# Performance work log

Measured on AMD Instinct MI355X. Metric: run time of the kernel, lower is better.

The kernel has to match this reference:

```python
import jax, jax.numpy as jnp
from jax import lax
import numpy as np

NUM_CLASSES = 21
CONF_THR = 0.01
NMS_THR = 0.45
TOP_K = 200
KEEP_TOP_K = 200
MIN_SIZES = [30., 60., 111., 162., 213., 264.]
MAX_SIZES = [60., 111., 162., 213., 264., 315.]
ASPECT_RATIOS = [[2.], [2., 3.], [2., 3.], [2., 3.], [2.], [2.]]
STEPS = [8., 16., 32., 64., 100., 300.]
VARIANCE = np.array([0.1, 0.1, 0.2, 0.2], np.float32)
CHANNELS = [512, 1024, 512, 256, 256, 256]
FEAT_HW = [38, 19, 10, 5, 3, 1]
IMG = 300.0
BATCH = 32


def _make_priors(i):
    # Caffe-style PriorBox: per cell -> [min, sqrt(min*max), ar & flipped ar boxes]
    fh = fw = FEAT_HW[i]
    m, M, step = MIN_SIZES[i], MAX_SIZES[i], STEPS[i]
    wh = [(m, m), (np.sqrt(m * M), np.sqrt(m * M))]
    for ar in ASPECT_RATIOS[i]:
        r = np.sqrt(ar)
        wh.append((m * r, m / r))
        wh.append((m / r, m * r))  # flip
    wh = np.asarray(wh, np.float32)                       # [np, 2]
    ys, xs = np.meshgrid(np.arange(fh), np.arange(fw), indexing='ij')
    cx = ((xs + 0.5) * step / IMG).astype(np.float32)     # [fh, fw]
    cy = ((ys + 0.5) * step / IMG).astype(np.float32)
    w = wh[:, 0] / IMG
    h = wh[:, 1] / IMG
    xmin = cx[..., None] - w * 0.5                        # [fh, fw, np]
    ymin = cy[..., None] - h * 0.5
    xmax = cx[..., None] + w * 0.5
    ymax = cy[..., None] + h * 0.5
    return np.stack([xmin, ymin, xmax, ymax], -1).reshape(-1, 4)


def _conv2d(x, w, b):
    y = lax.conv_general_dilated(x, w, (1, 1), 'SAME',
                                 dimension_numbers=('NCHW', 'OIHW', 'NCHW'))
    return y + b[None, :, None, None]


def _decode(loc, pri):
    # CENTER_SIZE decode with variance not encoded in target
    pw = pri[:, 2] - pri[:, 0]
    ph = pri[:, 3] - pri[:, 1]
    pcx = (pri[:, 0] + pri[:, 2]) * 0.5
    pcy = (pri[:, 1] + pri[:, 3]) * 0.5
    cx = pcx + VARIANCE[0] * loc[..., 0] * pw
    cy = pcy + VARIANCE[1] * loc[..., 1] * ph
    w = pw * jnp.exp(VARIANCE[2] * loc[..., 2])
    h = ph * jnp.exp(VARIANCE[3] * loc[..., 3])
    return jnp.stack([cx - w * 0.5, cy - h * 0.5, cx + w * 0.5, cy + h * 0.5], -1)


def _pairwise_iou(b):
    x1 = jnp.maximum(b[:, None, 0], b[None, :, 0])
    y1 = jnp.maximum(b[:, None, 1], b[None, :, 1])
    x2 = jnp.minimum(b[:, None, 2], b[None, :, 2])
    y2 = jnp.minimum(b[:, None, 3], b[None, :, 3])
    inter = jnp.clip(x2 - x1, 0.) * jnp.clip(y2 - y1, 0.)
    area = (b[:, 2] - b[:, 0]) * (b[:, 3] - b[:, 1])
    union = area[:, None] + area[None, :] - inter
    return inter / jnp.maximum(union, 1e-9)


def _nms_keep(iou, valid, thr):
    # sequential greedy suppression on score-sorted boxes (scan over rows)
    K = iou.shape[0]
    order = jnp.arange(K)
    def step(keep, i):
        sup = (iou[i] > thr) & (order > i) & keep[i]
        return keep & ~sup, None
    keep, _ = lax.scan(step, valid, order)
    return keep


def _per_image(boxes, conf, img_id):
    # boxes [P,4], conf [P,C]
    cls_scores = conf[:, 1:].T  # [C-1, P] (skip background class 0)
    def per_class(sc):
        s = jnp.where(sc > CONF_THR, sc, 0.)
        ts, idx = lax.top_k(s, TOP_K)
        b = boxes[idx]
        keep = _nms_keep(_pairwise_iou(b), ts > 0., NMS_THR)
        return jnp.where(keep, ts, 0.), b
    sc, bx = jax.vmap(per_class)(cls_scores)           # [C-1,K], [C-1,K,4]
    labels = jnp.repeat(jnp.arange(1, NUM_CLASSES), TOP_K).astype(jnp.float32)
    fs = sc.reshape(-1)
    fb = bx.reshape(-1, 4)
    ks, ki = lax.top_k(fs, KEEP_TOP_K)
    kb = fb[ki]
    kl = jnp.where(ks > 0., labels[ki], -1.)
    img_col = jnp.full((KEEP_TOP_K, 1), img_id, jnp.float32)
    return jnp.concatenate([img_col, kl[:, None], ks[:, None], kb], axis=1)  # [K,7]


PRIORS = jnp.asarray(np.concatenate([_make_priors(i) for i in range(6)], 0))  # [8732,4]


def setup_inputs():
    key = jax.random.key(0)
    ks = iter(jax.random.split(key, 64))
    d = {}
    for i, (c, hw) in enumerate(zip(CHANNELS, FEAT_HW)):
        d[f"feat{i}"] = jax.random.normal(next(ks), (BATCH, c, hw, hw), jnp.float32)
    d["img_tensor"] = jax.random.normal(next(ks), (BATCH, 3, 300, 300), jnp.float32)
    for i, c in enumerate(CHANNELS):
        npc = 2 + 2 * len(ASPECT_RATIOS[i])
        d[f"loc_w{i}"] = jax.random.normal(next(ks), (npc * 4, c, 3, 3), jnp.float32) * 0.01
        d[f"loc_b{i}"] = jnp.zeros((npc * 4,), jnp.float32)
        d[f"conf_w{i}"] = jax.random.normal(next(ks), (npc * NUM_CLASSES, c, 3, 3), jnp.float32) * 0.01
        d[f"conf_b{i}"] = jnp.zeros((npc * NUM_CLASSES,), jnp.float32)
    return d


def reference(feat0, feat1, feat2, feat3, feat4, feat5, img_tensor,
              loc_w0, loc_b0, conf_w0, conf_b0,
              loc_w1, loc_b1, conf_w1, conf_b1,
              loc_w2, loc_b2, conf_w2, conf_b2,
              loc_w3, loc_b3, conf_w3, conf_b3,
              loc_w4, loc_b4, conf_w4, conf_b4,
              loc_w5, loc_b5, conf_w5, conf_b5):
    feats = [feat0, feat1, feat2, feat3, feat4, feat5]
    lw = [loc_w0, loc_w1, loc_w2, loc_w3, loc_w4, loc_w5]
    lb = [loc_b0, loc_b1, loc_b2, loc_b3, loc_b4, loc_b5]
    cw = [conf_w0, conf_w1, conf_w2, conf_w3, conf_w4, conf_w5]
    cb = [conf_b0, conf_b1, conf_b2, conf_b3, conf_b4, conf_b5]
    B = feats[0].shape[0]
    locs, confs = [], []
    for i in range(6):
        # conv head -> NHWC -> flat, matching permute(0,2,3,1).view(B,-1)
        locs.append(_conv2d(feats[i], lw[i], lb[i]).transpose(0, 2, 3, 1).reshape(B, -1))
        confs.append(_conv2d(feats[i], cw[i], cb[i]).transpose(0, 2, 3, 1).reshape(B, -1))
    loc = jnp.concatenate(locs, 1).reshape(B, -1, 4)                       # [B,P,4]
    conf = jax.nn.softmax(jnp.concatenate(confs, 1).reshape(B, -1, NUM_CLASSES), -1)
    boxes = _decode(loc, PRIORS)                                           # [B,P,4]
    return jax.vmap(_per_image)(boxes, conf, jnp.arange(B, dtype=jnp.float32))  # [B,200,7]
```

## Files before the change

kernel.cpp:

```cpp
#include <hip/hip_runtime.h>
#include <math.h>

#define BATCH 32
#define P_TOTAL 8732


typedef __attribute__((ext_vector_type(8))) short bf16x8;
typedef __attribute__((ext_vector_type(4))) float f32x4;
typedef unsigned int uint;
typedef unsigned short ushort;

struct SQ {
  int C, logC, H, W, HW, M, ksteps, NL, N, npc, pbase, blkBase;
  int aOffB, wpkOffB, pauxOffB, biasOffB;
};
struct WPtrs { const float* lw[6]; const float* lb[6]; const float* cw[6]; const float* cb[6]; };
struct Tables { SQ sq[6]; int fillBase[6]; int fillTotal; int biasBase[6]; int biasTotal; };

__device__ __forceinline__ ushort f2bf(float f) {
  uint u = __float_as_uint(f);
  return (ushort)((u + 0x7FFFu + ((u >> 16) & 1u)) >> 16);
}
__device__ __forceinline__ float bf2f(ushort b) { return __uint_as_float(((uint)b) << 16); }

__global__ void make_priors(float* __restrict__ priors) {
  int p = blockIdx.x * 256 + threadIdx.x;
  if (p >= P_TOTAL) return;
  const int pb1 = 5776, pb2 = 7942, pb3 = 8542, pb4 = 8692, pb5 = 8728;
  int base, fw, npc;
  double m, M, st;
  if (p < pb1)      { base = 0;   fw = 38; npc = 4; m = 30.;  M = 60.;  st = 8.;   }
  else if (p < pb2) { base = pb1; fw = 19; npc = 6; m = 60.;  M = 111.; st = 16.;  }
  else if (p < pb3) { base = pb2; fw = 10; npc = 6; m = 111.; M = 162.; st = 32.;  }
  else if (p < pb4) { base = pb3; fw = 5;  npc = 6; m = 162.; M = 213.; st = 64.;  }
  else if (p < pb5) { base = pb4; fw = 3;  npc = 4; m = 213.; M = 264.; st = 100.; }
  else              { base = pb5; fw = 1;  npc = 4; m = 264.; M = 315.; st = 300.; }
  int lp = p - base;
  int cell = lp / npc, j = lp - cell * npc;
  int y = cell / fw, x = cell - y * fw;
  double w_, h_;
  if (j == 0)      { w_ = m; h_ = m; }
  else if (j == 1) { double ss = sqrt(m * M); w_ = ss; h_ = ss; }
  else {
    int q = j - 2;
    double r = sqrt((q < 2) ? 2.0 : 3.0);
    if ((q & 1) == 0) { w_ = m * r; h_ = m / r; }
    else              { w_ = m / r; h_ = m * r; }
  }
  float wf = (float)w_ / 300.0f;
  float hf = (float)h_ / 300.0f;
  float cx = (float)(((double)x + 0.5) * st / 300.0);
  float cy = (float)(((double)y + 0.5) * st / 300.0);
  float4 pr;
  pr.x = cx - wf * 0.5f; pr.y = cy - hf * 0.5f;
  pr.z = cx + wf * 0.5f; pr.w = cy + hf * 0.5f;
  ((float4*)priors)[p] = pr;
}

__global__ void nchw_to_nhwc(const float* __restrict__ in, float* __restrict__ out,
                             int C, int HW) {
  __shared__ float tile[32][33];
  int b = blockIdx.z;
  int hw0 = blockIdx.x * 32;
  int c0 = blockIdx.y * 32;
  int tx = threadIdx.x;
  int ty = threadIdx.y;
  const float* ip = in + (size_t)b * C * HW;
  float* op = out + (size_t)b * C * HW;
#pragma unroll
  for (int r = 0; r < 4; ++r) {
    int c = c0 + ty + 8 * r;
    int hw = hw0 + tx;
    tile[ty + 8 * r][tx] = (c < C && hw < HW) ? ip[(size_t)c * HW + hw] : 0.f;
  }
  __syncthreads();
#pragma unroll
  for (int r = 0; r < 4; ++r) {
    int hw = hw0 + ty + 8 * r;
    int c = c0 + tx;
    if (c < C && hw < HW) op[(size_t)hw * C + c] = tile[tx][ty + 8 * r];
  }
}

__global__ void zero_ws(uint4* __restrict__ p, long n) {
  uint4 z; z.x = z.y = z.z = z.w = 0u;
  for (long i = (long)blockIdx.x * 256 + threadIdx.x; i < n; i += (long)gridDim.x * 256)
    p[i] = z;
}

__global__ void wpk_fill(WPtrs wp, Tables tb, char* __restrict__ wsb) {
  int e = blockIdx.x * 256 + threadIdx.x;
  if (e >= tb.fillTotal) return;
  int s = 0;
#pragma unroll
  for (int i = 1; i < 6; ++i) if (e >= tb.fillBase[i]) s = i;
  SQ q = tb.sq[s];
  int le = e - tb.fillBase[s];
  int C8 = q.C >> 3;
  int n = le / C8, co = (le - n * C8) * 8;
  const float* src = (n < q.NL) ? (wp.lw[s] + ((size_t)n * q.C + co) * 9)
                                : (wp.cw[s] + ((size_t)(n - q.NL) * q.C + co) * 9);
  float v[72];
#pragma unroll
  for (int i = 0; i < 72; ++i) v[i] = src[i];
  int f = n >> 4, ln = n & 15;
  int g = (co & 31) >> 3;
  int NF = (q.N + 15) >> 4;
  char* wbase = wsb + q.wpkOffB;
#pragma unroll
  for (int tap = 0; tap < 9; ++tap) {
    int kb = (tap * q.C + co) >> 5;
    ushort h0[8], h1[8], h2[8];
#pragma unroll
    for (int i = 0; i < 8; ++i) {
      float a = v[i * 9 + tap];
      ushort a0 = f2bf(a); float t = a - bf2f(a0);
      ushort a1 = f2bf(t); float t2 = t - bf2f(a1);
      ushort a2 = f2bf(t2);
      h0[i] = a0; h1[i] = a1; h2[i] = a2;
    }
    char* d = wbase + (size_t)kb * NF * 3072 + f * 3072 + (g * 16 + ln) * 16;
    *(uint4*)(d)        = *(uint4*)h0;
    *(uint4*)(d + 1024) = *(uint4*)h1;
    *(uint4*)(d + 2048) = *(uint4*)h2;
  }
}

__global__ void bias_fill(WPtrs wp, Tables tb, char* __restrict__ wsb) {
  int e = blockIdx.x * 256 + threadIdx.x;
  if (e >= tb.biasTotal) return;
  int s = 0;
#pragma unroll
  for (int i = 1; i < 6; ++i) if (e >= tb.biasBase[i]) s = i;
  SQ q = tb.sq[s];
  int ln = e - tb.biasBase[s];
  float v = 0.f;
  if (ln < q.N) v = (ln < q.NL) ? wp.lb[s][ln] : wp.cb[s][ln - q.NL];
  ((float*)(wsb + q.biasOffB))[ln] = v;
}

__device__ __forceinline__ void split8(const float* vv, uint4& o0, uint4& o1, uint4& o2) {
  uint* a = (uint*)&o0; uint* b = (uint*)&o1; uint* c = (uint*)&o2;
#pragma unroll
  for (int i = 0; i < 4; ++i) {
    float x = vv[2 * i], y = vv[2 * i + 1];
    ushort x0 = f2bf(x); float xr = x - bf2f(x0);
    ushort x1 = f2bf(xr); ushort x2 = f2bf(xr - bf2f(x1));
    ushort y0 = f2bf(y); float yr = y - bf2f(y0);
    ushort y1 = f2bf(yr); ushort y2 = f2bf(yr - bf2f(y1));
    a[i] = (uint)x0 | ((uint)y0 << 16);
    b[i] = (uint)x1 | ((uint)y1 << 16);
    c[i] = (uint)x2 | ((uint)y2 << 16);
  }
}

template<int NF, bool PART>
__global__ __launch_bounds__(256, 2) void conv_mfma(const char* __restrict__ wsb,
                                                    SQ q0, SQ q1, SQ q2,
                                                    float* __restrict__ locbuf,
                                                    float* __restrict__ confbuf) {
  __shared__ char sm[30720 + NF * 3072];
  const int bid = blockIdx.x;
  SQ q = (bid >= q2.blkBase) ? q2 : ((bid >= q1.blkBase) ? q1 : q0);
  const int tid = threadIdx.x;
  const int C = q.C, W = q.W, H = q.H, HW = q.HW, M = q.M;
  int lb = bid - q.blkBase;
  int m0, kbeg, kend;
  if (PART) {
    m0 = (lb >> 1) * 128;
    int ks2 = q.ksteps >> 1;
    kbeg = (lb & 1) * ks2; kend = kbeg + ks2;
  } else {
    m0 = lb * 128; kbeg = 0; kend = q.ksteps;
  }
  const float* Amat = (const float*)(wsb + q.aOffB);
  const char* wpk = wsb + q.wpkOffB;

  const int r0 = tid >> 2, oct = tid & 3;
  int ry[2], rx[2], rrow[2];
  bool rv[2];
#pragma unroll
  for (int h = 0; h < 2; ++h) {
    int m = m0 + r0 + 64 * h;
    bool v = m < M;
    int mc = v ? m : 0;
    int b = mc / HW, rem = mc - b * HW;
    ry[h] = rem / W; rx[h] = rem - ry[h] * W; rrow[h] = b * H; rv[h] = v;
  }

  f32x4 cb[2][NF], ct[2][NF];
#pragma unroll
  for (int rf = 0; rf < 2; ++rf)
#pragma unroll
    for (int f = 0; f < NF; ++f) { cb[rf][f] = 0.f; ct[rf][f] = 0.f; }

  const int lane = tid & 63, wv = tid >> 6;
  const int ksub = q.logC - 5, kmask = (1 << ksub) - 1;
  int abase[2];
#pragma unroll
  for (int rf = 0; rf < 2; ++rf)
    abase[rf] = (32 * wv + 16 * rf + (lane & 15)) * 80 + (lane >> 4) * 16;

  for (int kb = kbeg; kb < kend; ++kb) {
    int tap = kb >> ksub;
    int c0 = (kb & kmask) << 5;
    int t3 = tap * 21846 >> 16;
    int dy = t3 - 1, dx = tap - t3 * 3 - 1;
    __syncthreads();
#pragma unroll
    for (int h = 0; h < 2; ++h) {
      int iy = ry[h] + dy, ix = rx[h] + dx;
      bool ok = rv[h] && (unsigned)iy < (unsigned)H && (unsigned)ix < (unsigned)W;
      float4 f0, f1;
      f0.x = f0.y = f0.z = f0.w = 0.f; f1 = f0;
      if (ok) {
        const float* p = Amat + (size_t)((rrow[h] + iy) * W + ix) * C + c0 + oct * 8;
        f0 = ((const float4*)p)[0]; f1 = ((const float4*)p)[1];
      }
      float vv[8] = {f0.x, f0.y, f0.z, f0.w, f1.x, f1.y, f1.z, f1.w};
      uint4 o0, o1, o2;
      split8(vv, o0, o1, o2);
      int ab = (r0 + 64 * h) * 80 + oct * 16;
      *(uint4*)(sm + ab)         = o0;
      *(uint4*)(sm + 10240 + ab) = o1;
      *(uint4*)(sm + 20480 + ab) = o2;
    }
    {
      const char* wsrc = wpk + (size_t)kb * (NF * 3072);
#pragma unroll
      for (int j = 0; j < (NF * 192 + 255) / 256; ++j) {
        int c = tid + j * 256;
        if (c < NF * 192) *(uint4*)(sm + 30720 + c * 16) = *(const uint4*)(wsrc + c * 16);
      }
    }
    __syncthreads();
    bf16x8 a0[2], a1[2], a2[2];
#pragma unroll
    for (int rf = 0; rf < 2; ++rf) {
      a0[rf] = *(const bf16x8*)(sm + abase[rf]);
      a1[rf] = *(const bf16x8*)(sm + 10240 + abase[rf]);
      a2[rf] = *(const bf16x8*)(sm + 20480 + abase[rf]);
    }
#pragma unroll
    for (int f = 0; f < NF; ++f) {
      const char* bp = sm + 30720 + f * 3072 + lane * 16;
      bf16x8 b0 = *(const bf16x8*)(bp);
      bf16x8 b1 = *(const bf16x8*)(bp + 1024);
      bf16x8 b2 = *(const bf16x8*)(bp + 2048);
#pragma unroll
      for (int rf = 0; rf < 2; ++rf) {
        cb[rf][f] = __builtin_amdgcn_mfma_f32_16x16x32_bf16(a0[rf], b0, cb[rf][f], 0, 0, 0);
        cb[rf][f] = __builtin_amdgcn_mfma_f32_16x16x32_bf16(a1[rf], b0, cb[rf][f], 0, 0, 0);
        cb[rf][f] = __builtin_amdgcn_mfma_f32_16x16x32_bf16(a0[rf], b1, cb[rf][f], 0, 0, 0);
        cb[rf][f] = __builtin_amdgcn_mfma_f32_16x16x32_bf16(a1[rf], b1, cb[rf][f], 0, 0, 0);
        cb[rf][f] = __builtin_amdgcn_mfma_f32_16x16x32_bf16(a2[rf], b0, cb[rf][f], 0, 0, 0);
        cb[rf][f] = __builtin_amdgcn_mfma_f32_16x16x32_bf16(a0[rf], b2, cb[rf][f], 0, 0, 0);
      }
    }
    if (((kb - kbeg) & 15) == 15 || kb == kend - 1) {
#pragma unroll
      for (int rf = 0; rf < 2; ++rf)
#pragma unroll
        for (int f = 0; f < NF; ++f) { ct[rf][f] += cb[rf][f]; cb[rf][f] = 0.f; }
    }
  }

  const float* bias = (const float*)(wsb + q.biasOffB);
#pragma unroll
  for (int rf = 0; rf < 2; ++rf) {
#pragma unroll
    for (int f = 0; f < NF; ++f) {
      int n = 16 * f + (lane & 15);
      if (n >= q.N) continue;
      int mrow = m0 + 32 * wv + 16 * rf + 4 * (lane >> 4);
      if (PART) {
        float* paux = (float*)(wsb + q.pauxOffB);
#pragma unroll
        for (int r = 0; r < 4; ++r) {
          int m = mrow + r;
          if (m < M) atomicAdd(&paux[(long)m * 160 + n], ct[rf][f][r]);
        }
      } else {
        float bv = bias[n];
#pragma unroll
        for (int r = 0; r < 4; ++r) {
          int m = mrow + r;
          if (m >= M) continue;
          float v = ct[rf][f][r] + bv;
          int b = m / HW, rem = m - b * HW;
          int pidx0 = q.pbase + rem * q.npc;
          if (n < q.NL) {
            locbuf[((long)b * P_TOTAL + pidx0 + (n >> 2)) * 4 + (n & 3)] = v;
          } else {
            int cn = n - q.NL;
            int pr = cn / 21, cl = cn - pr * 21;
            confbuf[((long)b * P_TOTAL + pidx0 + pr) * 21 + cl] = v;
          }
        }
      }
    }
  }
}

__global__ __launch_bounds__(256) void epi2(const char* __restrict__ wsb,
                                            SQ qa, SQ qb, SQ qc, int ta, int tb, int total,
                                            float* __restrict__ locbuf,
                                            float* __restrict__ confbuf) {
  int e = blockIdx.x * 256 + threadIdx.x;
  if (e >= total) return;
  SQ q; int le;
  if (e < ta) { q = qa; le = e; }
  else if (e < tb) { q = qb; le = e - ta; }
  else { q = qc; le = e - tb; }
  int m = le / q.N, n = le - m * q.N;
  float v = ((const float*)(wsb + q.pauxOffB))[(long)m * 160 + n]
          + ((const float*)(wsb + q.biasOffB))[n];
  int b = m / q.HW, rem = m - b * q.HW;
  int pidx0 = q.pbase + rem * q.npc;
  if (n < q.NL) {
    locbuf[((long)b * P_TOTAL + pidx0 + (n >> 2)) * 4 + (n & 3)] = v;
  } else {
    int cn = n - q.NL;
    int pr = cn / 21, cl = cn - pr * 21;
    confbuf[((long)b * P_TOTAL + pidx0 + pr) * 21 + cl] = v;
  }
}

__global__ __launch_bounds__(256) void decode_softmax(const float* __restrict__ locbuf,
                                                      const float* __restrict__ confbuf,
                                                      const float* __restrict__ priors,
                                                      float* __restrict__ boxes,
                                                      float* __restrict__ scores_t) {
  __shared__ float sc[20 * 256];
  int b = blockIdx.y;
  int p0 = blockIdx.x * 256;
  int tid = threadIdx.x;
  int p = p0 + tid;
  if (p < P_TOTAL) {
    long t = (long)b * P_TOTAL + p;
    float4 pri = ((const float4*)priors)[p];
    float4 lo = ((const float4*)locbuf)[t];
    float pw = pri.z - pri.x, ph = pri.w - pri.y;
    float pcx = (pri.x + pri.z) * 0.5f, pcy = (pri.y + pri.w) * 0.5f;
    float cx = pcx + 0.1f * lo.x * pw;
    float cy = pcy + 0.1f * lo.y * ph;
    float w = pw * expf(0.2f * lo.z);
    float h = ph * expf(0.2f * lo.w);
    float4 bx;
    bx.x = cx - w * 0.5f; bx.y = cy - h * 0.5f;
    bx.z = cx + w * 0.5f; bx.w = cy + h * 0.5f;
    ((float4*)boxes)[t] = bx;
    const float* cp = confbuf + t * 21;
    float l[21];
#pragma unroll
    for (int c = 0; c < 21; ++c) l[c] = cp[c];
    float mx = l[0];
#pragma unroll
    for (int c = 1; c < 21; ++c) mx = fmaxf(mx, l[c]);
    float e[21];
    float sum = 0.f;
#pragma unroll
    for (int c = 0; c < 21; ++c) { e[c] = expf(l[c] - mx); sum += e[c]; }
#pragma unroll
    for (int c = 1; c < 21; ++c) sc[(c - 1) * 256 + tid] = e[c] / sum;
  } else {
#pragma unroll
    for (int c = 0; c < 20; ++c) sc[c * 256 + tid] = 0.f;
  }
  __syncthreads();
  int np = min(256, P_TOTAL - p0);
  if (tid < np) {
    for (int c = 0; c < 20; ++c)
      scores_t[((long)b * 20 + c) * P_TOTAL + p0 + tid] = sc[c * 256 + tid];
  }
}

__global__ __launch_bounds__(256) void topk_nms(const float* __restrict__ scores_t,
                                                const float* __restrict__ boxes,
                                                float* __restrict__ pc_scores,
                                                float* __restrict__ pc_boxes) {
  int bc = blockIdx.x;
  int b = bc / 20;
  int tid = threadIdx.x;
  const float* sp = scores_t + (long)bc * P_TOTAL;

  float vals[35];
#pragma unroll
  for (int u = 0; u < 35; ++u) {
    int idx = u * 256 + tid;
    float v = -1.f;
    if (idx < P_TOTAL) {
      float s = sp[idx];
      v = (s > 0.01f) ? s : 0.f;
    }
    vals[u] = v;
  }

  __shared__ unsigned long long wred[4];
  __shared__ unsigned long long winner;
  __shared__ int sel_idx[200];
  __shared__ float sel_sc[200];
  __shared__ float bX1[200], bY1[200], bX2[200], bY2[200], bAr[200];

  for (int r = 0; r < 200; ++r) {
    float bv = vals[0]; int bu = 0;
#pragma unroll
// ... 60 lines not shown
            float yy1 = fmaxf(iy1, my1[s2]);
            float xx2 = fminf(ix2, mx2[s2]);
            float yy2 = fminf(iy2, my2[s2]);
            float inter = fmaxf(xx2 - xx1, 0.f) * fmaxf(yy2 - yy1, 0.f);
            float uni = fmaxf(ia + ma[s2] - inter, 1e-9f);
            if (inter / uni > 0.45f) km &= ~(1u << s2);
          }
        }
      }
    }
#pragma unroll
    for (int s2 = 0; s2 < 4; ++s2) {
      int j = tid + 64 * s2;
      if (j < 200) {
        long o = (long)bc * 200 + j;
        pc_scores[o] = ((km >> s2) & 1) ? sel_sc[j] : 0.f;
        float4 ob; ob.x = mx1[s2]; ob.y = my1[s2]; ob.z = mx2[s2]; ob.w = my2[s2];
        ((float4*)pc_boxes)[o] = ob;
      }
    }
  }
}

__global__ __launch_bounds__(256) void final_topk(const float* __restrict__ pc_scores,
                                                  const float* __restrict__ pc_boxes,
                                                  float* __restrict__ out) {
  int b = blockIdx.x;
  int tid = threadIdx.x;
  const float* fs = pc_scores + (long)b * 4000;
  float vals[16];
#pragma unroll
  for (int u = 0; u < 16; ++u) {
    int idx = u * 256 + tid;
    vals[u] = (idx < 4000) ? fs[idx] : -1.f;
  }
  __shared__ unsigned long long wred[4];
  __shared__ unsigned long long winner;
  __shared__ int kidx[200];
  __shared__ float ksc[200];
  for (int r = 0; r < 200; ++r) {
    float bv = vals[0]; int bu = 0;
#pragma unroll
    for (int u = 1; u < 16; ++u)
      if (vals[u] > bv) { bv = vals[u]; bu = u; }
    int bidx = bu * 256 + tid;
    unsigned long long key = (bv < 0.f) ? 0ull
        : (((unsigned long long)__float_as_uint(bv) << 32) | (unsigned)(0x7FFFFFFF - bidx));
#pragma unroll
    for (int off = 32; off > 0; off >>= 1) {
      unsigned long long o = __shfl_down(key, off);
      if (o > key) key = o;
    }
    if ((tid & 63) == 0) wred[tid >> 6] = key;
    __syncthreads();
    if (tid == 0) {
      unsigned long long k0 = wred[0];
      for (int w = 1; w < 4; ++w) if (wred[w] > k0) k0 = wred[w];
      winner = k0;
      kidx[r] = 0x7FFFFFFF - (int)(unsigned)(k0 & 0xFFFFFFFFu);
      ksc[r] = __uint_as_float((unsigned)(k0 >> 32));
    }
    __syncthreads();
    int wi = 0x7FFFFFFF - (int)(unsigned)(winner & 0xFFFFFFFFu);
    if ((wi & 255) == tid) {
      int u = wi >> 8;
#pragma unroll
      for (int uu = 0; uu < 16; ++uu) if (uu == u) vals[uu] = -1.f;
    }
    __syncthreads();
  }
  if (tid < 200) {
    int j = kidx[tid];
    float sc2 = ksc[tid];
    float4 bx = ((const float4*)pc_boxes)[(long)b * 4000 + j];
    float lab = (sc2 > 0.f) ? (float)(1 + j / 200) : -1.f;
    long o = ((long)b * 200 + tid) * 7;
    out[o + 0] = (float)b;
    out[o + 1] = lab;
    out[o + 2] = sc2;
    out[o + 3] = bx.x; out[o + 4] = bx.y; out[o + 5] = bx.z; out[o + 6] = bx.w;
  }
}

extern "C" void kernel_launch(void* const* d_in, const int* in_sizes, int n_in,
                              void* d_out, int out_size, void* d_ws, size_t ws_size,
                              hipStream_t stream) {
  (void)in_sizes; (void)n_in; (void)out_size; (void)ws_size;
  static const int CH[6]   = {512, 1024, 512, 256, 256, 256};
  static const int LOGC[6] = {9, 10, 9, 8, 8, 8};
  static const int FHW[6]  = {38, 19, 10, 5, 3, 1};
  static const int NPC[6]  = {4, 6, 6, 6, 4, 4};
  char* wsb = (char*)d_ws;
  Tables tb;
  WPtrs wp;
  auto al = [](size_t v) { return (v + 255) & ~(size_t)255; };
  size_t off = 0;
  int pb = 0;
  for (int s = 0; s < 6; ++s) {
    SQ& q = tb.sq[s];
    q.C = CH[s]; q.logC = LOGC[s]; q.H = FHW[s]; q.W = FHW[s];
    q.HW = FHW[s] * FHW[s];
    q.M = BATCH * q.HW;
    q.ksteps = CH[s] * 9 / 32;
    q.npc = NPC[s]; q.NL = NPC[s] * 4; q.N = NPC[s] * 25;
    q.pbase = pb; pb += q.HW * q.npc;
    q.aOffB = (int)off; off = al(off + (size_t)BATCH * q.HW * q.C * 4);
  }
  size_t zeroStart = off;
  for (int s = 0; s < 6; ++s) {
    int NF = (tb.sq[s].N + 15) >> 4;
    tb.sq[s].wpkOffB = (int)off;
    off = al(off + (size_t)tb.sq[s].ksteps * NF * 3072);
  }
  for (int s = 1; s <= 3; ++s) {
    tb.sq[s].pauxOffB = (int)off;
    off = al(off + (size_t)tb.sq[s].M * 160 * 4);
  }
  tb.sq[0].pauxOffB = tb.sq[4].pauxOffB = tb.sq[5].pauxOffB = 0;
  size_t zeroEnd = off;
  for (int s = 0; s < 6; ++s) {
    int NF = (tb.sq[s].N + 15) >> 4;
    tb.sq[s].biasOffB = (int)off;
    off = al(off + (size_t)NF * 16 * 4);
  }
  size_t priorsOffB = off; off = al(off + (size_t)P_TOTAL * 16);
  size_t locOffB    = off; off = al(off + (size_t)BATCH * P_TOTAL * 16);
  size_t confOffB   = off; off = al(off + (size_t)BATCH * P_TOTAL * 21 * 4);
  size_t boxesOffB  = off; off = al(off + (size_t)BATCH * P_TOTAL * 16);
  size_t scTOffB    = off; off = al(off + (size_t)BATCH * 20 * P_TOTAL * 4);
  size_t pcScOffB   = off; off = al(off + (size_t)BATCH * 20 * 200 * 4);
  size_t pcBxOffB   = off; off = al(off + (size_t)BATCH * 20 * 200 * 16);

  int fb = 0, bb = 0;
  for (int s = 0; s < 6; ++s) {
    tb.fillBase[s] = fb; fb += tb.sq[s].N * (tb.sq[s].C >> 3);
    tb.biasBase[s] = bb; bb += ((tb.sq[s].N + 15) >> 4) * 16;
  }
  tb.fillTotal = fb;
  tb.biasTotal = bb;

  for (int s = 0; s < 6; ++s) {
    wp.lw[s] = (const float*)d_in[7 + 4 * s];
    wp.lb[s] = (const float*)d_in[8 + 4 * s];
    wp.cw[s] = (const float*)d_in[9 + 4 * s];
    wp.cb[s] = (const float*)d_in[10 + 4 * s];
  }

  float* priors   = (float*)(wsb + priorsOffB);
  float* locbuf   = (float*)(wsb + locOffB);
  float* confbuf  = (float*)(wsb + confOffB);
  float* boxes    = (float*)(wsb + boxesOffB);
  float* scores_t = (float*)(wsb + scTOffB);
  float* pcSc     = (float*)(wsb + pcScOffB);
  float* pcBx     = (float*)(wsb + pcBxOffB);

  make_priors<<<(P_TOTAL + 255) / 256, 256, 0, stream>>>(priors);

  for (int s = 0; s < 6; ++s) {
    int hw = FHW[s] * FHW[s];
    dim3 g((hw + 31) / 32, (CH[s] + 31) / 32, BATCH);
    nchw_to_nhwc<<<g, dim3(32, 8), 0, stream>>>((const float*)d_in[s],
                                                (float*)(wsb + tb.sq[s].aOffB), CH[s], hw);
  }

  long zn = (long)((zeroEnd - zeroStart) >> 4);
  zero_ws<<<4096, 256, 0, stream>>>((uint4*)(wsb + zeroStart), zn);

  wpk_fill<<<(tb.fillTotal + 255) / 256, 256, 0, stream>>>(wp, tb, wsb);
  bias_fill<<<(tb.biasTotal + 255) / 256, 256, 0, stream>>>(wp, tb, wsb);

  {
    SQ q0 = tb.sq[0], q1 = tb.sq[4], q2 = tb.sq[5];
    q0.blkBase = 0;
    q1.blkBase = (q0.M + 127) / 128;
    q2.blkBase = q1.blkBase + (q1.M + 127) / 128;
    int grid = q2.blkBase + (q2.M + 127) / 128;
    conv_mfma<7, false><<<grid, 256, 0, stream>>>(wsb, q0, q1, q2, locbuf, confbuf);
  }
  {
    SQ q0 = tb.sq[1], q1 = tb.sq[2], q2 = tb.sq[3];
    q0.blkBase = 0;
    q1.blkBase = 2 * ((q0.M + 127) / 128);
    q2.blkBase = q1.blkBase + 2 * ((q1.M + 127) / 128);
    int grid = q2.blkBase + 2 * ((q2.M + 127) / 128);
    conv_mfma<10, true><<<grid, 256, 0, stream>>>(wsb, q0, q1, q2, locbuf, confbuf);
    int ta = q0.M * q0.N;
    int tbv = ta + q1.M * q1.N;
    int total = tbv + q2.M * q2.N;
    epi2<<<(total + 255) / 256, 256, 0, stream>>>(wsb, q0, q1, q2, ta, tbv, total,
                                                  locbuf, confbuf);
  }

  decode_softmax<<<dim3(35, BATCH), 256, 0, stream>>>(locbuf, confbuf, priors, boxes, scores_t);

  topk_nms<<<BATCH * 20, 256, 0, stream>>>(scores_t, boxes, pcSc, pcBx);

  final_topk<<<BATCH, 256, 0, stream>>>(pcSc, pcBx, (float*)d_out);
}
```

Baseline: 1.799 ms.

## Pre-split activations into bf16 planes and double-buffer weights in conv pipeline

The NCHW-to-NHWC transpose now also splits activations into three bf16 planes, so the MFMA conv kernel reads A fragments straight from global memory and no longer does per-step fp32 loads, splitting and shared-memory staging. Weight tiles are register-prefetched and double-buffered in shared memory, which removes one barrier per k-step. The split-K partial sums go to per-part buffers and are reduced by a single epilogue for all scales, which removes the atomics and the zeroing pass. The change also merges the bias fill into wpk_fill, uses magic-number divisions, splits K more finely for some scales, and reuses workspace regions. The cost is three times the activation-plane footprint and more global traffic for uncoalesced A loads.

Measured after the change: 2.075 ms. 1.15x slower.

```diff
diff --git a/kernel.cpp b/kernel.cpp
--- a/kernel.cpp
+++ b/kernel.cpp
@@ -11,11 +11,14 @@
 typedef unsigned short ushort;
 
 struct SQ {
-  int C, logC, H, W, HW, M, ksteps, NL, N, npc, pbase, blkBase;
-  int aOffB, wpkOffB, pauxOffB, biasOffB;
+  int C, H, W, HW, M, NL, N, npc, pbase;
+  int chunks, parts, mtiles, blkBase, nfw, epiBase, c8shift, fillBase, biasBase, tsBase, gx, nbi;
+  uint pmag, hwmag, wmag, nmag, tbmag, txmag;
+  long planeOffE, MC, wpkOffB, pauxOffF, biasOffF;
 };
+struct Tab { SQ q[6]; };
 struct WPtrs { const float* lw[6]; const float* lb[6]; const float* cw[6]; const float* cb[6]; };
-struct Tables { SQ sq[6]; int fillBase[6]; int fillTotal; int biasBase[6]; int biasTotal; };
+struct FP3 { const float* f0; const float* f1; const float* f2; };
 
 __device__ __forceinline__ ushort f2bf(float f) {
   uint u = __float_as_uint(f);
@@ -57,135 +60,131 @@
   ((float4*)priors)[p] = pr;
 }
 
-__global__ void nchw_to_nhwc(const float* __restrict__ in, float* __restrict__ out,
-                             int C, int HW) {
+__global__ __launch_bounds__(256) void transpose_split(FP3 fp, SQ qa, SQ qb, SQ qc,
+                                                       char* __restrict__ wsb) {
   __shared__ float tile[32][33];
-  int b = blockIdx.z;
-  int hw0 = blockIdx.x * 32;
-  int c0 = blockIdx.y * 32;
-  int tx = threadIdx.x;
-  int ty = threadIdx.y;
-  const float* ip = in + (size_t)b * C * HW;
-  float* op = out + (size_t)b * C * HW;
-#pragma unroll
-  for (int r = 0; r < 4; ++r) {
-    int c = c0 + ty + 8 * r;
+  int bid = blockIdx.x;
+  int sel = (bid >= qc.tsBase) ? 2 : (bid >= qb.tsBase) ? 1 : 0;
+  SQ q = (sel == 2) ? qc : (sel == 1) ? qb : qa;
+  const float* fsrc = (sel == 2) ? fp.f2 : (sel == 1) ? fp.f1 : fp.f0;
+  int local = bid - q.tsBase;
+  int b = __umulhi((uint)local, q.tbmag);
+  int r = local - b * q.nbi;
+  int cb_, hwb;
+  if (q.gx == 1) { cb_ = r; hwb = 0; }
+  else { cb_ = __umulhi((uint)r, q.txmag); hwb = r - cb_ * q.gx; }
+  int hw0 = hwb * 32, c0 = cb_ * 32;
+  int tx = threadIdx.x & 31, ty = threadIdx.x >> 5;
+  const float* ip = fsrc + (size_t)b * q.C * q.HW;
+#pragma unroll
+  for (int r2 = 0; r2 < 4; ++r2) {
+    int c = c0 + ty + 8 * r2;
     int hw = hw0 + tx;
-    tile[ty + 8 * r][tx] = (c < C && hw < HW) ? ip[(size_t)c * HW + hw] : 0.f;
+    tile[ty + 8 * r2][tx] = (hw < q.HW) ? ip[(size_t)c * q.HW + hw] : 0.f;
   }
   __syncthreads();
-#pragma unroll
-  for (int r = 0; r < 4; ++r) {
-    int hw = hw0 + ty + 8 * r;
+  ushort* p0 = (ushort*)wsb + q.planeOffE;
+  long MC = q.MC;
+#pragma unroll
+  for (int r2 = 0; r2 < 4; ++r2) {
+    int hw = hw0 + ty + 8 * r2;
     int c = c0 + tx;
-    if (c < C && hw < HW) op[(size_t)hw * C + c] = tile[tx][ty + 8 * r];
-  }
-}
-
-__global__ void zero_ws(uint4* __restrict__ p, long n) {
-  uint4 z; z.x = z.y = z.z = z.w = 0u;
-  for (long i = (long)blockIdx.x * 256 + threadIdx.x; i < n; i += (long)gridDim.x * 256)
-    p[i] = z;
-}
-
-__global__ void wpk_fill(WPtrs wp, Tables tb, char* __restrict__ wsb) {
+    if (hw < q.HW) {
+      float a = tile[tx][ty + 8 * r2];
+      ushort h0 = f2bf(a); float t = a - bf2f(h0);
+      ushort h1 = f2bf(t); ushort h2 = f2bf(t - bf2f(h1));
+      long o = ((long)b * q.HW + hw) * q.C + c;
+      p0[o] = h0; p0[o + MC] = h1; p0[o + 2 * MC] = h2;
+    }
+  }
+}
+
+__global__ __launch_bounds__(256) void wpk_fill(WPtrs wp, Tab tb, char* __restrict__ wsb,
+                                                int fillTotal, int total) {
   int e = blockIdx.x * 256 + threadIdx.x;
-  if (e >= tb.fillTotal) return;
-  int s = 0;
-#pragma unroll
-  for (int i = 1; i < 6; ++i) if (e >= tb.fillBase[i]) s = i;
-  SQ q = tb.sq[s];
-  int le = e - tb.fillBase[s];
-  int C8 = q.C >> 3;
-  int n = le / C8, co = (le - n * C8) * 8;
-  const float* src = (n < q.NL) ? (wp.lw[s] + ((size_t)n * q.C + co) * 9)
-                                : (wp.cw[s] + ((size_t)(n - q.NL) * q.C + co) * 9);
-  float v[72];
-#pragma unroll
-  for (int i = 0; i < 72; ++i) v[i] = src[i];
-  int f = n >> 4, ln = n & 15;
-  int g = (co & 31) >> 3;
-  int NF = (q.N + 15) >> 4;
-  char* wbase = wsb + q.wpkOffB;
-#pragma unroll
-  for (int tap = 0; tap < 9; ++tap) {
-    int kb = (tap * q.C + co) >> 5;
-    ushort h0[8], h1[8], h2[8];
-#pragma unroll
-    for (int i = 0; i < 8; ++i) {
-      float a = v[i * 9 + tap];
-      ushort a0 = f2bf(a); float t = a - bf2f(a0);
-      ushort a1 = f2bf(t); float t2 = t - bf2f(a1);
-      ushort a2 = f2bf(t2);
-      h0[i] = a0; h1[i] = a1; h2[i] = a2;
-    }
-    char* d = wbase + (size_t)kb * NF * 3072 + f * 3072 + (g * 16 + ln) * 16;
-    *(uint4*)(d)        = *(uint4*)h0;
-    *(uint4*)(d + 1024) = *(uint4*)h1;
-    *(uint4*)(d + 2048) = *(uint4*)h2;
-  }
-}
-
-__global__ void bias_fill(WPtrs wp, Tables tb, char* __restrict__ wsb) {
-  int e = blockIdx.x * 256 + threadIdx.x;
-  if (e >= tb.biasTotal) return;
-  int s = 0;
-#pragma unroll
-  for (int i = 1; i < 6; ++i) if (e >= tb.biasBase[i]) s = i;
-  SQ q = tb.sq[s];
-  int ln = e - tb.biasBase[s];
-  float v = 0.f;
-  if (ln < q.N) v = (ln < q.NL) ? wp.lb[s][ln] : wp.cb[s][ln - q.NL];
-  ((float*)(wsb + q.biasOffB))[ln] = v;
-}
-
-__device__ __forceinline__ void split8(const float* vv, uint4& o0, uint4& o1, uint4& o2) {
-  uint* a = (uint*)&o0; uint* b = (uint*)&o1; uint* c = (uint*)&o2;
-#pragma unroll
-  for (int i = 0; i < 4; ++i) {
-    float x = vv[2 * i], y = vv[2 * i + 1];
-    ushort x0 = f2bf(x); float xr = x - bf2f(x0);
-    ushort x1 = f2bf(xr); ushort x2 = f2bf(xr - bf2f(x1));
-    ushort y0 = f2bf(y); float yr = y - bf2f(y0);
-    ushort y1 = f2bf(yr); ushort y2 = f2bf(yr - bf2f(y1));
-    a[i] = (uint)x0 | ((uint)y0 << 16);
-    b[i] = (uint)x1 | ((uint)y1 << 16);
-    c[i] = (uint)x2 | ((uint)y2 << 16);
-  }
-}
-
-template<int NF, bool PART>
-__global__ __launch_bounds__(256, 2) void conv_mfma(const char* __restrict__ wsb,
-                                                    SQ q0, SQ q1, SQ q2,
-                                                    float* __restrict__ locbuf,
-                                                    float* __restrict__ confbuf) {
-  __shared__ char sm[30720 + NF * 3072];
+  if (e >= total) return;
+  if (e < fillTotal) {
+    int s = 0;
+#pragma unroll
+    for (int i = 1; i < 6; ++i) if (e >= tb.q[i].fillBase) s = i;
+    SQ q = tb.q[s];
+    int le = e - q.fillBase;
+    int C8 = q.C >> 3;
+    int n = le >> q.c8shift;
+    int co = (le & (C8 - 1)) << 3;
+    int f = n >> 4, ln = n & 15, g = (co & 31) >> 3;
+    int NF = q.nfw >> 4;
+    char* wb = wsb + q.wpkOffB;
+    bool realn = n < q.N;
+    const float* src = realn ? ((n < q.NL) ? wp.lw[s] + ((size_t)n * q.C + co) * 9
+                                           : wp.cw[s] + ((size_t)(n - q.NL) * q.C + co) * 9)
+                             : (const float*)0;
+#pragma unroll
+    for (int tap = 0; tap < 9; ++tap) {
+      int kb = (co >> 5) * 9 + tap;
+      ushort h0[8], h1[8], h2[8];
+#pragma unroll
+      for (int i = 0; i < 8; ++i) {
+        float a = realn ? src[i * 9 + tap] : 0.f;
+        ushort a0 = f2bf(a); float t = a - bf2f(a0);
+        ushort a1 = f2bf(t); ushort a2 = f2bf(t - bf2f(a1));
+        h0[i] = a0; h1[i] = a1; h2[i] = a2;
+      }
+      char* d = wb + (size_t)kb * (NF * 3072) + f * 3072 + (g * 16 + ln) * 16;
+      *(uint4*)(d)        = *(uint4*)h0;
+      *(uint4*)(d + 1024) = *(uint4*)h1;
+      *(uint4*)(d + 2048) = *(uint4*)h2;
+    }
+  } else {
+    int e2 = e - fillTotal;
+    int s = 0;
+#pragma unroll
+    for (int i = 1; i < 6; ++i) if (e2 >= tb.q[i].biasBase) s = i;
+    SQ q = tb.q[s];
+    int ln = e2 - q.biasBase;
+    float v = 0.f;
+    if (ln < q.N) v = (ln < q.NL) ? wp.lb[s][ln] : wp.cb[s][ln - q.NL];
+    ((float*)wsb + q.biasOffF)[ln] = v;
+  }
+}
+
+template<int NF>
+__global__ __launch_bounds__(256, 2) void conv_mfma(char* __restrict__ wsb,
+                                                    SQ q0, SQ q1, SQ q2) {
+  __shared__ __attribute__((aligned(16))) char smB[2 * NF * 3072];
   const int bid = blockIdx.x;
-  SQ q = (bid >= q2.blkBase) ? q2 : ((bid >= q1.blkBase) ? q1 : q0);
-  const int tid = threadIdx.x;
-  const int C = q.C, W = q.W, H = q.H, HW = q.HW, M = q.M;
+  SQ q = (bid >= q2.blkBase) ? q2 : (bid >= q1.blkBase) ? q1 : q0;
   int lb = bid - q.blkBase;
-  int m0, kbeg, kend;
-  if (PART) {
-    m0 = (lb >> 1) * 128;
-    int ks2 = q.ksteps >> 1;
-    kbeg = (lb & 1) * ks2; kend = kbeg + ks2;
-  } else {
-    m0 = lb * 128; kbeg = 0; kend = q.ksteps;
-  }
-  const float* Amat = (const float*)(wsb + q.aOffB);
-  const char* wpk = wsb + q.wpkOffB;
-
-  const int r0 = tid >> 2, oct = tid & 3;
-  int ry[2], rx[2], rrow[2];
-  bool rv[2];
-#pragma unroll
-  for (int h = 0; h < 2; ++h) {
-    int m = m0 + r0 + 64 * h;
-    bool v = m < M;
-    int mc = v ? m : 0;
-    int b = mc / HW, rem = mc - b * HW;
-    ry[h] = rem / W; rx[h] = rem - ry[h] * W; rrow[h] = b * H; rv[h] = v;
+  int mt, part;
+  if (q.parts == 1) { mt = lb; part = 0; }
+  else { mt = __umulhi((uint)lb, q.pmag); part = lb - mt * q.parts; }
+  const int m0 = mt << 7;
+  int cbeg, cend;
+  if (q.parts == 1) { cbeg = 0; cend = q.chunks; }
+  else {
+    cbeg = __umulhi((uint)(part * q.chunks), q.pmag);
+    cend = __umulhi((uint)((part + 1) * q.chunks), q.pmag);
+  }
+  const int tid = threadIdx.x, lane = tid & 63, wv = tid >> 6;
+  const int colf = lane & 15, koct = lane >> 4;
+  const ushort* plane0 = (const ushort*)wsb + q.planeOffE;
+  const long MC = q.MC;
+
+  int yv[2], xv[2], mvalid[2];
+  long pixoff[2];
+#pragma unroll
+  for (int rf = 0; rf < 2; ++rf) {
+    int m = m0 + 32 * wv + 16 * rf + colf;
+    int valid = (m < q.M);
+    int mc = valid ? m : 0;
+    int b, rem;
+    if (q.HW == 1) { b = mc; rem = 0; }
+    else { b = __umulhi((uint)mc, q.hwmag); rem = mc - b * q.HW; }
+    int y, x;
+    if (q.W == 1) { y = rem; x = 0; }
+    else { y = __umulhi((uint)rem, q.wmag); x = rem - y * q.W; }
+    yv[rf] = y; xv[rf] = x; mvalid[rf] = valid;
+    pixoff[rf] = ((long)(b * q.H + y) * q.W + x) * q.C + koct * 8;
   }
 
   f32x4 cb[2][NF], ct[2][NF];
@@ -194,59 +193,49 @@
 #pragma unroll
     for (int f = 0; f < NF; ++f) { cb[rf][f] = 0.f; ct[rf][f] = 0.f; }
 
-  const int lane = tid & 63, wv = tid >> 6;
-  const int ksub = q.logC - 5, kmask = (1 << ksub) - 1;
-  int abase[2];
-#pragma unroll
-  for (int rf = 0; rf < 2; ++rf)
-    abase[rf] = (32 * wv + 16 * rf + (lane & 15)) * 80 + (lane >> 4) * 16;
-
+  const int SEG = NF * 192;
+  constexpr int NSTG = (NF * 192 + 255) / 256;
+  uint4 stg[NSTG];
+  const char* wpkb = wsb + q.wpkOffB;
+  const int kbeg = cbeg * 9, kend = cend * 9;
+  {
+    const uint4* s4 = (const uint4*)(wpkb + (size_t)kbeg * (NF * 3072));
+#pragma unroll
+    for (int j = 0; j < NSTG; ++j) { int c = tid + j * 256; if (c < SEG) stg[j] = s4[c]; }
+  }
+  int cur = 0, chunk = cbeg, tap = 0;
   for (int kb = kbeg; kb < kend; ++kb) {
-    int tap = kb >> ksub;
-    int c0 = (kb & kmask) << 5;
-    int t3 = tap * 21846 >> 16;
+    {
+      uint4* d = (uint4*)(smB + cur * (NF * 3072));
+#pragma unroll
+      for (int j = 0; j < NSTG; ++j) { int c = tid + j * 256; if (c < SEG) d[c] = stg[j]; }
+    }
+    __syncthreads();
+    if (kb + 1 < kend) {
+      const uint4* s4 = (const uint4*)(wpkb + (size_t)(kb + 1) * (NF * 3072));
+#pragma unroll
+      for (int j = 0; j < NSTG; ++j) { int c = tid + j * 256; if (c < SEG) stg[j] = s4[c]; }
+    }
+    int t3 = (tap * 43) >> 7;
     int dy = t3 - 1, dx = tap - t3 * 3 - 1;
-    __syncthreads();
-#pragma unroll
-    for (int h = 0; h < 2; ++h) {
-      int iy = ry[h] + dy, ix = rx[h] + dx;
-      bool ok = rv[h] && (unsigned)iy < (unsigned)H && (unsigned)ix < (unsigned)W;
-      float4 f0, f1;
-      f0.x = f0.y = f0.z = f0.w = 0.f; f1 = f0;
-      if (ok) {
-        const float* p = Amat + (size_t)((rrow[h] + iy) * W + ix) * C + c0 + oct * 8;
-        f0 = ((const float4*)p)[0]; f1 = ((const float4*)p)[1];
-      }
-      float vv[8] = {f0.x, f0.y, f0.z, f0.w, f1.x, f1.y, f1.z, f1.w};
-      uint4 o0, o1, o2;
-      split8(vv, o0, o1, o2);
-      int ab = (r0 + 64 * h) * 80 + oct * 16;
-      *(uint4*)(sm + ab)         = o0;
-      *(uint4*)(sm + 10240 + ab) = o1;
-      *(uint4*)(sm + 20480 + ab) = o2;
-    }
-    {
-      const char* wsrc = wpk + (size_t)kb * (NF * 3072);
-#pragma unroll
-      for (int j = 0; j < (NF * 192 + 255) / 256; ++j) {
-        int c = tid + j * 256;
-        if (c < NF * 192) *(uint4*)(sm + 30720 + c * 16) = *(const uint4*)(wsrc + c * 16);
-      }
-    }
-    __syncthreads();
+    long soff = (long)(dy * q.W + dx) * q.C + (chunk << 5);
     bf16x8 a0[2], a1[2], a2[2];
 #pragma unroll
     for (int rf = 0; rf < 2; ++rf) {
-      a0[rf] = *(const bf16x8*)(sm + abase[rf]);
-      a1[rf] = *(const bf16x8*)(sm + 10240 + abase[rf]);
-      a2[rf] = *(const bf16x8*)(sm + 20480 + abase[rf]);
-    }
+      int ok = mvalid[rf] & ((uint)(yv[rf] + dy) < (uint)q.H) & ((uint)(xv[rf] + dx) < (uint)q.W);
+      const ushort* ap = plane0 + (pixoff[rf] + soff);
+      uint4 v0 = *(const uint4*)(ap);
+      uint4 v1 = *(const uint4*)(ap + MC);
+      uint4 v2 = *(const uint4*)(ap + 2 * MC);
+      if (!ok) { v0.x = v0.y = v0.z = v0.w = 0u; v1 = v0; v2 = v0; }
+      a0[rf] = *(bf16x8*)&v0; a1[rf] = *(bf16x8*)&v1; a2[rf] = *(bf16x8*)&v2;
+    }
+    const char* bb = smB + cur * (NF * 3072) + lane * 16;
 #pragma unroll
     for (int f = 0; f < NF; ++f) {
-      const char* bp = sm + 30720 + f * 3072 + lane * 16;
-      bf16x8 b0 = *(const bf16x8*)(bp);
-      bf16x8 b1 = *(const bf16x8*)(bp + 1024);
-      bf16x8 b2 = *(const bf16x8*)(bp + 2048);
+      bf16x8 b0 = *(const bf16x8*)(bb + f * 3072);
+      bf16x8 b1 = *(const bf16x8*)(bb + f * 3072 + 1024);
+      bf16x8 b2 = *(const bf16x8*)(bb + f * 3072 + 2048);
 #pragma unroll
       for (int rf = 0; rf < 2; ++rf) {
         cb[rf][f] = __builtin_amdgcn_mfma_f32_16x16x32_bf16(a0[rf], b0, cb[rf][f], 0, 0, 0);
@@ -257,71 +246,57 @@
         cb[rf][f] = __builtin_amdgcn_mfma_f32_16x16x32_bf16(a0[rf], b2, cb[rf][f], 0, 0, 0);
       }
     }
-    if (((kb - kbeg) & 15) == 15 || kb == kend - 1) {
+    if (tap == 8) {
 #pragma unroll
       for (int rf = 0; rf < 2; ++rf)
 #pragma unroll
         for (int f = 0; f < NF; ++f) { ct[rf][f] += cb[rf][f]; cb[rf][f] = 0.f; }
     }
-  }
-
-  const float* bias = (const float*)(wsb + q.biasOffB);
-#pragma unroll
-  for (int rf = 0; rf < 2; ++rf) {
+    cur ^= 1;
+    if (++tap == 9) { tap = 0; ++chunk; }
+  }
+
+  float* paux = (float*)wsb + q.pauxOffF + (long)part * q.M * q.nfw;
+#pragma unroll
+  for (int rf = 0; rf < 2; ++rf)
 #pragma unroll
     for (int f = 0; f < NF; ++f) {
-      int n = 16 * f + (lane & 15);
-      if (n >= q.N) continue;
-      int mrow = m0 + 32 * wv + 16 * rf + 4 * (lane >> 4);
-      if (PART) {
-        float* paux = (float*)(wsb + q.pauxOffB);
-#pragma unroll
-        for (int r = 0; r < 4; ++r) {
-          int m = mrow + r;
-          if (m < M) atomicAdd(&paux[(long)m * 160 + n], ct[rf][f][r]);
-        }
-      } else {
-        float bv = bias[n];
-#pragma unroll
-        for (int r = 0; r < 4; ++r) {
-          int m = mrow + r;
-          if (m >= M) continue;
-          float v = ct[rf][f][r] + bv;
-          int b = m / HW, rem = m - b * HW;
-          int pidx0 = q.pbase + rem * q.npc;
-          if (n < q.NL) {
-            locbuf[((long)b * P_TOTAL + pidx0 + (n >> 2)) * 4 + (n & 3)] = v;
-          } else {
-            int cn = n - q.NL;
-            int pr = cn / 21, cl = cn - pr * 21;
-            confbuf[((long)b * P_TOTAL + pidx0 + pr) * 21 + cl] = v;
-          }
-        }
+      int n = f * 16 + colf;
+      int mr = m0 + 32 * wv + 16 * rf + 4 * koct;
+#pragma unroll
+      for (int r = 0; r < 4; ++r) {
+        int m = mr + r;
+        if (m < q.M) paux[(long)m * q.nfw + n] = ct[rf][f][r];
       }
     }
-  }
-}
-
-__global__ __launch_bounds__(256) void epi2(const char* __restrict__ wsb,
-                                            SQ qa, SQ qb, SQ qc, int ta, int tb, int total,
-                                            float* __restrict__ locbuf,
-                                            float* __restrict__ confbuf) {
-  int e = blockIdx.x * 256 + threadIdx.x;
-  if (e >= total) return;
-  SQ q; int le;
-  if (e < ta) { q = qa; le = e; }
-  else if (e < tb) { q = qb; le = e - ta; }
-  else { q = qc; le = e - tb; }
-  int m = le / q.N, n = le - m * q.N;
-  float v = ((const float*)(wsb + q.pauxOffB))[(long)m * 160 + n]
-          + ((const float*)(wsb + q.biasOffB))[n];
-  int b = m / q.HW, rem = m - b * q.HW;
+}
+
+__global__ __launch_bounds__(256) void epi(const char* __restrict__ wsb, Tab tb,
+                                           float* __restrict__ locbuf,
+                                           float* __restrict__ confbuf) {
+  int bid = blockIdx.x;
+  int s = 0;
+#pragma unroll
+  for (int i = 1; i < 6; ++i) if (bid >= tb.q[i].epiBase) s = i;
+  SQ q = tb.q[s];
+  int e = (bid - q.epiBase) * 256 + threadIdx.x;
+  if (e >= q.M * q.N) return;
+  int m = __umulhi((uint)e, q.nmag);
+  int n = e - m * q.N;
+  const float* pa = (const float*)wsb + q.pauxOffF + (long)m * q.nfw + n;
+  float v = ((const float*)wsb + q.biasOffF)[n];
+  long pstride = (long)q.M * q.nfw;
+  for (int p = 0; p < q.parts; ++p) v += pa[p * pstride];
+  int b, rem;
+  if (q.HW == 1) { b = m; rem = 0; }
+  else { b = __umulhi((uint)m, q.hwmag); rem = m - b * q.HW; }
   int pidx0 = q.pbase + rem * q.npc;
   if (n < q.NL) {
     locbuf[((long)b * P_TOTAL + pidx0 + (n >> 2)) * 4 + (n & 3)] = v;
   } else {
     int cn = n - q.NL;
-    int pr = cn / 21, cl = cn - pr * 21;
+    int pr = __umulhi((uint)cn, 204522253u);
+    int cl = cn - pr * 21;
     confbuf[((long)b * P_TOTAL + pidx0 + pr) * 21 + cl] = v;
   }
 }
@@ -548,62 +523,106 @@
   }
 }
 
+static inline uint magu(uint d) { return (uint)((0x100000000ull + d - 1) / d); }
+static inline size_t al256(size_t v) { return (v + 255) & ~(size_t)255; }
+
 extern "C" void kernel_launch(void* const* d_in, const int* in_sizes, int n_in,
                               void* d_out, int out_size, void* d_ws, size_t ws_size,
                               hipStream_t stream) {
   (void)in_sizes; (void)n_in; (void)out_size; (void)ws_size;
-  static const int CH[6]   = {512, 1024, 512, 256, 256, 256};
-  static const int LOGC[6] = {9, 10, 9, 8, 8, 8};
-  static const int FHW[6]  = {38, 19, 10, 5, 3, 1};
-  static const int NPC[6]  = {4, 6, 6, 6, 4, 4};
+  static const int CH[6]    = {512, 1024, 512, 256, 256, 256};
+  static const int FHW[6]   = {38, 19, 10, 5, 3, 1};
+  static const int NPC[6]   = {4, 6, 6, 6, 4, 4};
+  static const int PARTS[6] = {2, 4, 4, 2, 2, 1};
+  static const int GRPA[3] = {0, 4, 5};
+  static const int GRPB[3] = {1, 2, 3};
   char* wsb = (char*)d_ws;
-  Tables tb;
+  Tab tb;
   WPtrs wp;
-  auto al = [](size_t v) { return (v + 255) & ~(size_t)255; };
-  size_t off = 0;
   int pb = 0;
   for (int s = 0; s < 6; ++s) {
-    SQ& q = tb.sq[s];
-    q.C = CH[s]; q.logC = LOGC[s]; q.H = FHW[s]; q.W = FHW[s];
-    q.HW = FHW[s] * FHW[s];
+    SQ& q = tb.q[s];
+    q.C = CH[s]; q.H = FHW[s]; q.W = FHW[s]; q.HW = FHW[s] * FHW[s];
     q.M = BATCH * q.HW;
-    q.ksteps = CH[s] * 9 / 32;
     q.npc = NPC[s]; q.NL = NPC[s] * 4; q.N = NPC[s] * 25;
+    q.nfw = ((q.N + 15) >> 4) << 4;
     q.pbase = pb; pb += q.HW * q.npc;
-    q.aOffB = (int)off; off = al(off + (size_t)BATCH * q.HW * q.C * 4);
-  }
-  size_t zeroStart = off;
+    q.chunks = q.C >> 5;
+    q.parts = PARTS[s];
+    q.mtiles = (q.M + 127) >> 7;
+    q.pmag = (q.parts >= 2) ? magu((uint)q.parts) : 0;
+    q.hwmag = (q.HW >= 2) ? magu((uint)q.HW) : 0;
+    q.wmag = (q.W >= 2) ? magu((uint)q.W) : 0;
+    q.nmag = magu((uint)q.N);
+    q.MC = (long)q.M * q.C;
+    int c8 = q.C >> 3;
+    q.c8shift = (c8 == 128) ? 7 : (c8 == 64) ? 6 : 5;
+  }
+  size_t off = 0;
   for (int s = 0; s < 6; ++s) {
-    int NF = (tb.sq[s].N + 15) >> 4;
-    tb.sq[s].wpkOffB = (int)off;
-    off = al(off + (size_t)tb.sq[s].ksteps * NF * 3072);
-  }
-  for (int s = 1; s <= 3; ++s) {
-    tb.sq[s].pauxOffB = (int)off;
-    off = al(off + (size_t)tb.sq[s].M * 160 * 4);
-  }
-  tb.sq[0].pauxOffB = tb.sq[4].pauxOffB = tb.sq[5].pauxOffB = 0;
-  size_t zeroEnd = off;
+    SQ& q = tb.q[s];
+    int NF = q.nfw >> 4;
+    q.wpkOffB = (long)off;
+    off = al256(off + (size_t)(q.chunks * 9) * NF * 3072);
+  }
   for (int s = 0; s < 6; ++s) {
-    int NF = (tb.sq[s].N + 15) >> 4;
-    tb.sq[s].biasOffB = (int)off;
-    off = al(off + (size_t)NF * 16 * 4);
-  }
-  size_t priorsOffB = off; off = al(off + (size_t)P_TOTAL * 16);
-  size_t locOffB    = off; off = al(off + (size_t)BATCH * P_TOTAL * 16);
-  size_t confOffB   = off; off = al(off + (size_t)BATCH * P_TOTAL * 21 * 4);
-  size_t boxesOffB  = off; off = al(off + (size_t)BATCH * P_TOTAL * 16);
-  size_t scTOffB    = off; off = al(off + (size_t)BATCH * 20 * P_TOTAL * 4);
-  size_t pcScOffB   = off; off = al(off + (size_t)BATCH * 20 * 200 * 4);
-  size_t pcBxOffB   = off; off = al(off + (size_t)BATCH * 20 * 200 * 16);
-
-  int fb = 0, bb = 0;
+    SQ& q = tb.q[s];
+    q.biasOffF = (long)(off >> 2);
+    off = al256(off + (size_t)q.nfw * 4);
+  }
+  size_t priorsOffB = off; off = al256(off + (size_t)P_TOTAL * 16);
+
+  size_t Ab = off;
+  size_t ca = Ab;
+  for (int gi = 0; gi < 3; ++gi) {
+    SQ& q = tb.q[GRPA[gi]];
+    q.planeOffE = (long)(ca >> 1);
+    ca = al256(ca + (size_t)3 * q.MC * 2);
+  }
+  size_t endPlanesA = ca;
+  size_t cb2 = Ab;
+  for (int gi = 0; gi < 3; ++gi) {
+    SQ& q = tb.q[GRPB[gi]];
+    q.planeOffE = (long)(cb2 >> 1);
+    cb2 = al256(cb2 + (size_t)3 * q.MC * 2);
+  }
+  for (int gi = 0; gi < 3; ++gi) {
+    SQ& q = tb.q[GRPB[gi]];
+    q.pauxOffF = (long)(cb2 >> 2);
+    cb2 = al256(cb2 + (size_t)q.parts * q.M * q.nfw * 4);
+  }
+  size_t endB2 = cb2;
+  size_t locOffB   = Ab;
+  size_t confOffB  = al256(locOffB + (size_t)BATCH * P_TOTAL * 16);
+  size_t boxesOffB = al256(confOffB + (size_t)BATCH * P_TOTAL * 21 * 4);
+  size_t endLCB    = al256(boxesOffB + (size_t)BATCH * P_TOTAL * 16);
+  size_t Aend = endPlanesA;
+  if (endB2 > Aend) Aend = endB2;
+  if (endLCB > Aend) Aend = endLCB;
+
+  size_t Bb = al256(Aend);
+  size_t cc = Bb;
+  for (int gi = 0; gi < 3; ++gi) {
+    SQ& q = tb.q[GRPA[gi]];
+    q.pauxOffF = (long)(cc >> 2);
+    cc = al256(cc + (size_t)q.parts * q.M * q.nfw * 4);
+  }
+  size_t scTOffB  = Bb;
+  size_t pcScOffB = al256(scTOffB + (size_t)BATCH * 20 * P_TOTAL * 4);
+  size_t pcBxOffB = al256(pcScOffB + (size_t)BATCH * 20 * 200 * 4);
+
+  int fb = 0, bb2 = 0, eb = 0;
   for (int s = 0; s < 6; ++s) {
-    tb.fillBase[s] = fb; fb += tb.sq[s].N * (tb.sq[s].C >> 3);
-    tb.biasBase[s] = bb; bb += ((tb.sq[s].N + 15) >> 4) * 16;
-  }
-  tb.fillTotal = fb;
-  tb.biasTotal = bb;
+    SQ& q = tb.q[s];
+    q.fillBase = fb; fb += q.nfw * (q.C >> 3);
+    q.biasBase = bb2; bb2 += q.nfw;
+    q.epiBase = eb; eb += (q.M * q.N + 255) >> 8;
+    q.gx = (q.HW + 31) >> 5;
+    q.nbi = q.gx * (q.C >> 5);
+    q.tbmag = magu((uint)q.nbi);
+    q.txmag = (q.gx >= 2) ? magu((uint)q.gx) : 0;
+  }
+  int fillTotal = fb, wpkTotal = fb + bb2, epiBlocks = eb;
 
   for (int s = 0; s < 6; ++s) {
     wp.lw[s] = (const float*)d_in[7 + 4 * s];
@@ -621,41 +640,38 @@
   float* pcBx     = (float*)(wsb + pcBxOffB);
 
   make_priors<<<(P_TOTAL + 255) / 256, 256, 0, stream>>>(priors);
-
-  for (int s = 0; s < 6; ++s) {
-    int hw = FHW[s] * FHW[s];
-    dim3 g((hw + 31) / 32, (CH[s] + 31) / 32, BATCH);
-    nchw_to_nhwc<<<g, dim3(32, 8), 0, stream>>>((const float*)d_in[s],
-                                                (float*)(wsb + tb.sq[s].aOffB), CH[s], hw);
-  }
-
-  long zn = (long)((zeroEnd - zeroStart) >> 4);
-  zero_ws<<<4096, 256, 0, stream>>>((uint4*)(wsb + zeroStart), zn);
-
-  wpk_fill<<<(tb.fillTotal + 255) / 256, 256, 0, stream>>>(wp, tb, wsb);
-  bias_fill<<<(tb.biasTotal + 255) / 256, 256, 0, stream>>>(wp, tb, wsb);
+  wpk_fill<<<(wpkTotal + 255) / 256, 256, 0, stream>>>(wp, tb, wsb, fillTotal, wpkTotal);
 
   {
-    SQ q0 = tb.sq[0], q1 = tb.sq[4], q2 = tb.sq[5];
-    q0.blkBase = 0;
-    q1.blkBase = (q0.M + 127) / 128;
-    q2.blkBase = q1.blkBase + (q1.M + 127) / 128;
-    int grid = q2.blkBase + (q2.M + 127) / 128;
-    conv_mfma<7, false><<<grid, 256, 0, stream>>>(wsb, q0, q1, q2, locbuf, confbuf);
+    SQ qa = tb.q[0], qb = tb.q[4], qc = tb.q[5];
+    qa.tsBase = 0;
+    qb.tsBase = qa.nbi * BATCH;
+    qc.tsBase = qb.tsBase + qb.nbi * BATCH;
+    int tgrid = qc.tsBase + qc.nbi * BATCH;
+    FP3 f3; f3.f0 = (const float*)d_in[0]; f3.f1 = (const float*)d_in[4]; f3.f2 = (const float*)d_in[5];
+    transpose_split<<<tgrid, 256, 0, stream>>>(f3, qa, qb, qc, wsb);
+    qa.blkBase = 0;
+    qb.blkBase = qa.mtiles * qa.parts;
+    qc.blkBase = qb.blkBase + qb.mtiles * qb.parts;
+    int grid = qc.blkBase + qc.mtiles * qc.parts;
+    conv_mfma<7><<<grid, 256, 0, stream>>>(wsb, qa, qb, qc);
   }
   {
-    SQ q0 = tb.sq[1], q1 = tb.sq[2], q2 = tb.sq[3];
-    q0.blkBase = 0;
-    q1.blkBase = 2 * ((q0.M + 127) / 128);
-    q2.blkBase = q1.blkBase + 2 * ((q1.M + 127) / 128);
-    int grid = q2.blkBase + 2 * ((q2.M + 127) / 128);
-    conv_mfma<10, true><<<grid, 256, 0, stream>>>(wsb, q0, q1, q2, locbuf, confbuf);
-    int ta = q0.M * q0.N;
-    int tbv = ta + q1.M * q1.N;
-    int total = tbv + q2.M * q2.N;
-    epi2<<<(total + 255) / 256, 256, 0, stream>>>(wsb, q0, q1, q2, ta, tbv, total,
-                                                  locbuf, confbuf);
-  }
+    SQ qa = tb.q[1], qb = tb.q[2], qc = tb.q[3];
+    qa.tsBase = 0;
+    qb.tsBase = qa.nbi * BATCH;
+    qc.tsBase = qb.tsBase + qb.nbi * BATCH;
+    int tgrid = qc.tsBase + qc.nbi * BATCH;
+    FP3 f3; f3.f0 = (const float*)d_in[1]; f3.f1 = (const float*)d_in[2]; f3.f2 = (const float*)d_in[3];
+    transpose_split<<<tgrid, 256, 0, stream>>>(f3, qa, qb, qc, wsb);
+    qa.blkBase = 0;
+    qb.blkBase = qa.mtiles * qa.parts;
+    qc.blkBase = qb.blkBase + qb.mtiles * qb.parts;
+    int grid = qc.blkBase + qc.mtiles * qc.parts;
+    conv_mfma<10><<<grid, 256, 0, stream>>>(wsb, qa, qb, qc);
+  }
+
+  epi<<<epiBlocks, 256, 0, stream>>>(wsb, tb, locbuf, confbuf);
 
   decode_softmax<<<dim3(35, BATCH), 256, 0, stream>>>(locbuf, confbuf, priors, boxes, scores_t);
 
```
